# Optimization experiments

Measured on AMD Instinct MI355X. Metric: run time of the kernel, lower is better.

## Reference

```python
import jax, jax.numpy as jnp
import numpy as np

EPS = 1e-8
CG_TOL = 1e-4
S_SIGMA = 8   # bilateral grid spatial downsampling
N_BINS = 9    # bilateral grid range bins (intensity in [0,1])


def _conv2d(x, k):
    # x [C,H,W], k [kh,kw] -> same-padded cross-correlation, per channel
    kh, kw = k.shape
    out = jax.lax.conv_general_dilated(x[:, None], k[None, None], (1, 1),
                                       [(kh // 2, kh // 2), (kw // 2, kw // 2)])
    return out[:, 0]


def _conv2d_T(x, k):
    return _conv2d(x, k[::-1, ::-1])


def _conv_bank(x, ks):
    # x [C,H,W], ks [N,kh,kw] -> [N,C,H,W]
    n, kh, kw = ks.shape
    out = jax.lax.conv_general_dilated(x[:, None], ks[:, None], (1, 1),
                                       [(kh // 2, kh // 2), (kw // 2, kw // 2)])
    return out.transpose(1, 0, 2, 3)


def _conv_bank_T(v, ks):
    # v [N,C,H,W] -> sum_n conv(v[n], flip(ks[n])) : [C,H,W]
    n, kh, kw = ks.shape
    lhs = v.transpose(1, 0, 2, 3)          # [C,N,H,W]
    rhs = ks[:, ::-1, ::-1][None]          # [1,N,kh,kw]
    out = jax.lax.conv_general_dilated(lhs, rhs, (1, 1),
                                       [(kh // 2, kh // 2), (kw // 2, kw // 2)])
    return out[:, 0]


def _deconv_grad(blurred, x, kernel, dkw, dks, rkw, rks, rpow, reg_targets):
    # gradient of E(x) = sum_i dkw_i ||dk_i * (k*x - b)||^2
    #                  + sum_j rkw_j sum |rk_j*x - t_j|^{p_j}
    Kx = _conv2d(x, kernel) - blurred
    d = _conv_bank(Kx, dks)                                    # [Nd,C,H,W]
    g = _conv2d_T(_conv_bank_T(2.0 * dkw[:, None, None, None] * d, dks), kernel)
    v = _conv_bank(x, rks) - reg_targets                       # [Nr,C,H,W]
    av = jnp.abs(v) + EPS
    phi = jnp.sign(v) * av ** (rpow[:, None, None, None] - 1.0)
    g = g + _conv_bank_T(rkw[:, None, None, None] * rpow[:, None, None, None] * phi, rks)
    return g


def _deconv_alpha(blurred, x, kernel, dkw, dks, rkw, rks, rpow, reg_targets, p):
    # exact line search for the quadratic part, Gauss-Newton for |.|^p prior
    g = _deconv_grad(blurred, x, kernel, dkw, dks, rkw, rks, rpow, reg_targets)
    num = -jnp.sum(g * p)
    Kp = _conv2d(p, kernel)
    dKp = _conv_bank(Kp, dks)
    den = jnp.sum(2.0 * dkw[:, None, None, None] * dKp ** 2)
    v = _conv_bank(x, rks) - reg_targets
    Rp = _conv_bank(p, rks)
    w = (rkw * rpow * (rpow - 1.0))[:, None, None, None]
    den = den + jnp.sum(w * (jnp.abs(v) + EPS) ** (rpow[:, None, None, None] - 2.0) * Rp ** 2)
    return num / (den + 1e-12)


def _deconv_prior(x, rks, thr):
    # soft-shrinkage of filtered responses -> regularization targets
    v = _conv_bank(x, rks)
    return jnp.sign(v) * jnp.maximum(jnp.abs(v) - thr[:, None, None, None], 0.0)


def _conv_axis(g, f, axis):
    k = f.shape[0]; r = k // 2; L = g.shape[axis]
    pad = [(0, 0)] * g.ndim; pad[axis] = (r, r)
    gp = jnp.pad(g, pad)
    out = jnp.zeros_like(g)
    for t in range(k):  # fixed small tap count
        out = out + f[t] * jax.lax.slice_in_dim(gp, t, t + L, axis=axis)
    return out


def _bilateral_channel(I, fs, fr):
    # learned-filter bilateral grid: splat -> separable filter (fs,fs,fr) -> trilinear slice
    H, W = I.shape
    gh, gw = H // S_SIGMA, W // S_SIGMA
    Ic = jnp.clip(I, 0.0, 1.0)
    yy, xx = jnp.meshgrid(jnp.arange(H), jnp.arange(W), indexing="ij")
    yi = yy // S_SIGMA; xi = xx // S_SIGMA
    zi = jnp.clip(jnp.round(Ic * (N_BINS - 1)).astype(jnp.int32), 0, N_BINS - 1)
    flat = ((yi * gw + xi) * N_BINS + zi).ravel()
    gv = jnp.zeros(gh * gw * N_BINS, Ic.dtype).at[flat].add(Ic.ravel())
    gw_ = jnp.zeros(gh * gw * N_BINS, Ic.dtype).at[flat].add(1.0)
    g2 = jnp.stack([gv, gw_], -1).reshape(gh, gw, N_BINS, 2)
    g2 = _conv_axis(_conv_axis(_conv_axis(g2, fs, 0), fs, 1), fr, 2)
    yf = yy / S_SIGMA; xf = xx / S_SIGMA; zf = Ic * (N_BINS - 1)

    def corners(f, n):
        c0 = jnp.clip(jnp.floor(f).astype(jnp.int32), 0, n - 1)
        c1 = jnp.minimum(c0 + 1, n - 1)
        w = jnp.clip(f - c0, 0.0, 1.0)
        return c0, c1, w

    y0, y1, wy = corners(yf, gh)
    x0, x1, wx = corners(xf, gw)
    z0, z1, wz = corners(zf, N_BINS)
    acc = jnp.zeros(I.shape + (2,), Ic.dtype)
    for yc, wyc in ((y0, 1 - wy), (y1, wy)):
        for xc, wxc in ((x0, 1 - wx), (x1, wx)):
            for zc, wzc in ((z0, 1 - wz), (z1, wz)):
                acc = acc + (wyc * wxc * wzc)[..., None] * g2[yc, xc, zc]
    return acc[..., 0] / (acc[..., 1] + 1e-8)


def _forward(blurred_batch, kernel_batch, data_kernels, data_kernel_weights,
             reg_kernels, reg_kernel_weights, reg_powers, filter_s, filter_r,
             reg_thresholds, num_cg_iter):
    num_stages = filter_s.shape[0]
    n_reg = reg_kernels.shape[1]

    def single(blurred, kernel):
        def cg(x, idx, reg_targets):
            dkw = data_kernel_weights[idx]; dks = data_kernels[idx]
            rkw = reg_kernel_weights[idx]; rks = reg_kernels[idx]; rp = reg_powers[idx]
            g = _deconv_grad(blurred, x, kernel, dkw, dks, rkw, rks, rp, reg_targets)
            r = -g
            r_norm = jnp.sum(r * r)
            r0 = r_norm

            def body(i, carry):
                x, r, p, rn, done = carry
                alpha = _deconv_alpha(blurred, x, kernel, dkw, dks, rkw, rks, rp, reg_targets, p)
                x1 = x + alpha * p
                g1 = _deconv_grad(blurred, x1, kernel, dkw, dks, rkw, rks, rp, reg_targets)
                r1 = -g1
                nrn = jnp.sum(r1 * r1)
                beta = nrn / (rn + 1e-20)
                conv_now = nrn < CG_TOL * r0
                p1 = r1 + beta * p
                x_n = jnp.where(done, x, x1)
                r_n = jnp.where(done, r, r1)
                rn_n = jnp.where(done, rn, nrn)
                p_n = jnp.where(done | conv_now, p, p1)
                return (x_n, r_n, p_n, rn_n, done | conv_now)

            carry = (x, r, r, r_norm, jnp.array(False))
            x, _, _, _, _ = jax.lax.fori_loop(0, num_cg_iter, body, carry)
            return x

        x = cg(blurred, 0, jnp.zeros((n_reg,) + blurred.shape, blurred.dtype))
        for stage in range(num_stages):
            x = jax.vmap(lambda ch: _bilateral_channel(ch, filter_s[stage], filter_r[stage]))(x)
            reg_targets = _deconv_prior(x, reg_kernels[stage + 1], reg_thresholds[stage])
            x = cg(x, stage + 1, reg_targets)
        return x

    return jax.vmap(single)(blurred_batch, kernel_batch)


def setup_inputs() -> dict:
    key = jax.random.key(0)
    k1, k2 = jax.random.split(key)
    B, C, H, W, KS = 2, 3, 512, 512, 15
    blurred = jax.random.uniform(k1, (B, C, H, W), jnp.float32)
    kern = jax.random.uniform(k2, (B, KS, KS), jnp.float32)
    kern = kern / jnp.sum(kern, axis=(1, 2), keepdims=True)  # normalized PSFs

    ns = 1; c = 2  # num_stages, kernel center (5x5)
    rk = np.zeros((ns + 1, 5, 5, 5), np.float32)
    rk[:, 0, c, c] = -1.0; rk[:, 0, c + 1, c] = 1.0
    rk[:, 1, c, c] = -1.0; rk[:, 1, c, c + 1] = 1.0
    rk[:, 2, c, c] = 1.0; rk[:, 2, c + 1, c] = -1.0
    rk[:, 2, c, c + 1] = -1.0; rk[:, 2, c + 1, c + 1] = 1.0
    rk[:, 3, c - 1, c] = 1.0; rk[:, 3, c, c] = -2.0; rk[:, 3, c + 1, c] = 1.0
    rk[:, 4, c, c - 1] = 1.0; rk[:, 4, c, c] = -2.0; rk[:, 4, c, c + 1] = 1.0
    dk = np.zeros((ns + 1, 6, 5, 5), np.float32)
    dk[:, 0, c, c] = 1.0
    dk[:, 1:] = rk
    dkw = np.zeros((ns + 1, 6), np.float32); dkw[:, 0] = 1.0
    rkw = np.zeros((ns + 1, 5), np.float32)
    rkw[0, :] = 0.001; rkw[1:, :] = 0.05
    rpow = np.full((ns + 1, 5), 2.0, np.float32)
    fs = np.zeros((ns, 11), np.float32); fs[:, 3:8] = [0.0, 1.0, 2.0, 1.0, 0.0]
    fr = np.tile(np.array([0.0, 1.0, 2.0, 1.0, 0.0], np.float32), (ns, 1))
    thr = np.tile(np.array([0.065, 0.065, 0.0325, 0.0325, 0.0325], np.float32), (ns, 1))

    return {
        "blurred_batch": blurred,
        "kernel_batch": kern,
        "data_kernels": jnp.asarray(dk),
        "data_kernel_weights": jnp.asarray(dkw),
        "reg_kernels": jnp.asarray(rk),
        "reg_kernel_weights": jnp.asarray(rkw),
        "reg_powers": jnp.asarray(rpow),
        "filter_s": jnp.asarray(fs),
        "filter_r": jnp.asarray(fr),
        "reg_thresholds": jnp.asarray(thr),
        "num_cg_iter": 5,
    }


def reference(blurred_batch, kernel_batch, data_kernels, data_kernel_weights,
              reg_kernels, reg_kernel_weights, reg_powers, filter_s, filter_r,
              reg_thresholds, num_cg_iter):
    return _forward(blurred_batch, kernel_batch, data_kernels, data_kernel_weights,
                    reg_kernels, reg_kernel_weights, reg_powers, filter_s, filter_r,
                    reg_thresholds, num_cg_iter)
```

## Files before the change

kernel.cpp:

```cpp
#include <hip/hip_runtime.h>

constexpr int Bn = 2, Cn = 3, Hh = 512, Ww = 512;
constexpr int KS = 15, KR = 7;
constexpr int NDK = 6, NRK = 5;
constexpr int GH = 64, GW = 64, NBn = 9, SS = 8;
constexpr float EPSf = 1e-8f;
constexpr float CGTOL = 1e-4f;
constexpr int PLANE = Hh * Ww;
constexpr int CHW = Cn * PLANE;
constexpr int BX = 64, BY = 16;
constexpr int GXc = Ww / BX, GYc = Hh / BY;
constexpr int PB = GXc * GYc * Cn;
constexpr int SA = 80, THt = 30;
constexpr int S2W = 72, S2H = 24;
constexpr int PHW = 68, PHH = 20;
constexpr int PHG = (PHW / 4) * PHH;
constexpr int NITER = 5;

struct CgState { float alpha, beta, rn, r0; int done, pflag; int pad0, pad1; };

struct SolveInfo {
    int fastBank;
    int allrp2;
    int nd;
// ... 38 lines not shown
                    acc += ch * rks_i[m * 25 + ay * 5 + ax] * rks_i[m * 25 + by * 5 + bx];
                }
        }
        s->C[t] = acc;
    }
    if (t == 81) {
        int fast = 1, nd = 0; float tot = 0.f;
        for (int n = 0; n < NDK; n++) {
            if (dkw_i[n] == 0.f) continue;
            int cnt = 0, pos = -1;
            for (int q = 0; q < 25; q++) if (dks_i[n * 25 + q] != 0.f) { cnt++; pos = q; }
            if (cnt > 1) fast = 0;
            if (cnt == 1 && nd < NDK) {
                float v = dks_i[n * 25 + pos];
                s->dsc[nd] = 2.f * dkw_i[n] * v * v;
                s->ddy[nd] = pos / 5 - 2; s->ddx[nd] = pos % 5 - 2;
                tot += s->dsc[nd]; nd++;
            }
        }
        s->fastBank = fast; s->nd = fast ? nd : 0; s->sctot = tot;
    }
    if (t == 82) {
        int ok = 1;
        for (int m = 0; m < NRK; m++) {
            float wm = rkw_i[m], rp = rpw_i[m];
            if (wm != 0.f && rp != 2.f && wm * rp * (rp - 1.f) != 0.f) ok = 0;
        }
        s->allrp2 = ok;
    }
}

__global__ __launch_bounds__(256)
void k_conv15(const float* __restrict__ src, const float* __restrict__ rb,
              const float* __restrict__ pbuf, float* __restrict__ xcopy,
              const float* __restrict__ sub, float* __restrict__ out,
              const float* __restrict__ kernB, float* __restrict__ part,
              const SolveInfo* __restrict__ si,
              const CgState* __restrict__ st, const int* __restrict__ ncg,
              int iter, int mode)
{
    const int pz = blockIdx.z, b = pz / Cn, c = pz % Cn;
    const CgState s = st[b];
    if (mode == 2 && (s.done != 0 || iter >= *ncg)) return;
    __shared__ __align__(16) float tile[SA * THt];
    __shared__ float red[256];
    const int tx = threadIdx.x, ty = threadIdx.y, tid = ty * 16 + tx;
    const int ox0 = blockIdx.x * BX, oy0 = blockIdx.y * BY;
    const int baseP = pz * PLANE;
    const float beta = s.beta; const int pf = s.pflag;
    const float* kp = kernB + b * 225;

    float nm = 0.f;
    for (int i = tid; i < 78 * THt; i += 256) {
        int ly = i / 78, lx = i % 78;
        int gy = oy0 - KR + ly, gx = ox0 - KR + lx;
        float v = 0.f;
        if (gy >= 0 && gy < Hh && gx >= 0 && gx < Ww) {
            int gi = baseP + gy * Ww + gx;
            if (mode == 2) {
                float rv = rb[gi], pv = pbuf[gi];
                v = pf ? fmaf(beta, pv, rv) : pv;
                if (ly >= KR && ly < KR + BY && lx >= KR && lx < KR + BX)
                    nm = fmaf(rv, v, nm);
            } else {
                v = src[gi];
                if (mode == 0 && ly >= KR && ly < KR + BY && lx >= KR && lx < KR + BX)
                    xcopy[gi] = v;
            }
        }
        tile[ly * SA + lx] = v;
    }
    __syncthreads();

    const int colbase = tx * 4;
    float a0 = 0.f, a1 = 0.f, a2 = 0.f, a3 = 0.f;
    for (int i = 0; i < KS; i++) {
        const float4* rp4 = reinterpret_cast<const float4*>(&tile[(ty + i) * SA + colbase]);
        float f[20];
        #pragma unroll
        for (int s5 = 0; s5 < 5; s5++) {
            float4 w4 = rp4[s5];
            f[s5 * 4] = w4.x; f[s5 * 4 + 1] = w4.y; f[s5 * 4 + 2] = w4.z; f[s5 * 4 + 3] = w4.w;
        }
        const float* kr = kp + i * 15;
        #pragma unroll
        for (int j = 0; j < KS; j++) {
            float kv = kr[j];
            a0 = fmaf(kv, f[j], a0); a1 = fmaf(kv, f[j + 1], a1);
            a2 = fmaf(kv, f[j + 2], a2); a3 = fmaf(kv, f[j + 3], a3);
        }
    }
    const int gi = baseP + (oy0 + ty) * Ww + ox0 + colbase;
    if (sub) {
        float4 sv = *reinterpret_cast<const float4*>(&sub[gi]);
        a0 -= sv.x; a1 -= sv.y; a2 -= sv.z; a3 -= sv.w;
    }
    if (si->fastBank) {
        const int gy = oy0 + ty, gx0 = ox0 + colbase;
        if (gy >= 2 && gy <= Hh - 3 && gx0 >= 2 && gx0 + 3 <= Ww - 3) {
            float sc = si->sctot;
// ... 83 lines not shown
            if (!gyin || gx0 + 3 < 0 || gx0 + 3 >= Ww) v3 = 0.f;
            *reinterpret_cast<float4*>(&dl[zy * PHW + zx0]) = make_float4(v0, v1, v2, v3);
        }
        __syncthreads();
        float c0 = 0.f, c1 = 0.f, c2 = 0.f, c3 = 0.f;
        #pragma unroll
        for (int a = 0; a < 5; a++) {
            int fr = 4 - a;
            bool rz = dnr[fr*5]==0.f && dnr[fr*5+1]==0.f && dnr[fr*5+2]==0.f &&
                      dnr[fr*5+3]==0.f && dnr[fr*5+4]==0.f;
            if (rz) continue;
            const float4* q4 = reinterpret_cast<const float4*>(&dl[(ty + a) * PHW + colbase]);
            float4 u0 = q4[0], u1 = q4[1];
            float f8[8] = {u0.x,u0.y,u0.z,u0.w,u1.x,u1.y,u1.z,u1.w};
            #pragma unroll
            for (int bb = 0; bb < 5; bb++) {
                float kv = dnr[fr * 5 + (4 - bb)];
                if (kv != 0.f) {
                    c0 = fmaf(kv, f8[bb], c0); c1 = fmaf(kv, f8[bb+1], c1);
                    c2 = fmaf(kv, f8[bb+2], c2); c3 = fmaf(kv, f8[bb+3], c3);
                }
            }
        }
        t0 = fmaf(wn, c0, t0); t1 = fmaf(wn, c1, t1);
        t2 = fmaf(wn, c2, t2); t3 = fmaf(wn, c3, t3);
        __syncthreads();
    }
    const int gi = baseP + (oy0 + ty) * Ww + ox0 + colbase;
    *reinterpret_cast<float4*>(&tbuf[gi]) = make_float4(t0, t1, t2, t3);
}

__global__ __launch_bounds__(256)
void k_hess(const float* __restrict__ kx, const float* __restrict__ wb,
            const float* __restrict__ rb, const float* __restrict__ pbuf,
            float* __restrict__ qb, const float* __restrict__ kernB,
            const float* __restrict__ rks, const float* __restrict__ rkw,
            const float* __restrict__ rpw, const SolveInfo* __restrict__ si,
            float* __restrict__ part, const CgState* __restrict__ st,
            const int* __restrict__ ncg, int iter)
{
    if (!si->allrp2) return;
    const int pz = blockIdx.z, b = pz / Cn, c = pz % Cn;
    const CgState s = st[b];
    if (s.done != 0 || iter >= *ncg) return;
    __shared__ __align__(16) float wt[SA * THt];
    __shared__ __align__(16) float s2[S2W * S2H];
    __shared__ __align__(16) float sC[81];
    __shared__ float rk5[NRK * 25];
    __shared__ float srkw[NRK], srpw[NRK];
    __shared__ float red[256];
    float* ph = wt;
    const int tx = threadIdx.x, ty = threadIdx.y, tid = ty * 16 + tx;
    const int ox0 = blockIdx.x * BX, oy0 = blockIdx.y * BY;
    const int baseP = pz * PLANE;
    const float beta = s.beta; const int pf = s.pflag;
    const float* wsrc = si->fastBank ? kx : wb;
    const float* kp = kernB + b * 225;

    for (int i = tid; i < 81; i += 256) sC[i] = si->C[i];
    for (int i = tid; i < NRK * 25; i += 256) rk5[i] = rks[i];
    if (tid < NRK) { srkw[tid] = rkw[tid]; srpw[tid] = rpw[tid]; }

    for (int i = tid; i < 78 * THt; i += 256) {
        int ly = i / 78, lx = i % 78;
        int gy = oy0 - KR + ly, gx = ox0 - KR + lx;
        wt[ly * SA + lx] = (gy >= 0 && gy < Hh && gx >= 0 && gx < Ww)
                           ? wsrc[baseP + gy * Ww + gx] : 0.f;
    }
    for (int i = tid; i < S2W * S2H; i += 256) {
        int ly = i / S2W, lx = i % S2W;
        int gy = oy0 - 4 + ly, gx = ox0 - 4 + lx;
        float v = 0.f;
        if (gy >= 0 && gy < Hh && gx >= 0 && gx < Ww) {
            int gi = baseP + gy * Ww + gx;
            float rv = rb[gi], pv = pbuf[gi];
            v = pf ? fmaf(beta, pv, rv) : pv;
        }
        s2[i] = v;
    }
    __syncthreads();

    const int colbase = tx * 4;
    float a0 = 0.f, a1 = 0.f, a2 = 0.f, a3 = 0.f;
    for (int i = 0; i < KS; i++) {
        const float4* rp4 = reinterpret_cast<const float4*>(&wt[(ty + i) * SA + colbase]);
        float f[20];
        #pragma unroll
        for (int s5 = 0; s5 < 5; s5++) {
            float4 w4 = rp4[s5];
            f[s5 * 4] = w4.x; f[s5 * 4 + 1] = w4.y; f[s5 * 4 + 2] = w4.z; f[s5 * 4 + 3] = w4.w;
        }
        const float* kr = kp + (14 - i) * 15;
        #pragma unroll
        for (int j = 0; j < KS; j++) {
            float kv = kr[14 - j];
            a0 = fmaf(kv, f[j], a0); a1 = fmaf(kv, f[j + 1], a1);
            a2 = fmaf(kv, f[j + 2], a2); a3 = fmaf(kv, f[j + 3], a3);
        }
    }

    const bool blkInterior = (oy0 >= 2) && (oy0 + BY - 1 <= Hh - 3) &&
                             (ox0 >= 2) && (ox0 + BX - 1 <= Ww - 3);
    if (blkInterior) {
        #pragma unroll
        for (int oy = 0; oy < 9; oy++) {
            float cr[9]; bool nz = false;
            #pragma unroll
            for (int ox = 0; ox < 9; ox++) { cr[ox] = sC[oy * 9 + ox]; nz = nz || (cr[ox] != 0.f); }
            if (!nz) continue;
            const float4* s4 = reinterpret_cast<const float4*>(&s2[(ty + oy) * S2W + colbase]);
            float4 u0 = s4[0], u1 = s4[1], u2 = s4[2];
// ... 54 lines not shown
                if (rz) continue;
                const float4* q4 = reinterpret_cast<const float4*>(&ph[(ty + a) * PHW + colbase]);
                float4 u0 = q4[0], u1 = q4[1];
                float f8[8] = {u0.x,u0.y,u0.z,u0.w,u1.x,u1.y,u1.z,u1.w};
                #pragma unroll
                for (int bb = 0; bb < 5; bb++) {
                    float kv = rmr[fr * 5 + (4 - bb)];
                    if (kv != 0.f) {
                        a0 = fmaf(kv, f8[bb], a0); a1 = fmaf(kv, f8[bb+1], a1);
                        a2 = fmaf(kv, f8[bb+2], a2); a3 = fmaf(kv, f8[bb+3], a3);
                    }
                }
            }
            __syncthreads();
        }
    }

    const int gy = oy0 + ty, gx0 = ox0 + colbase;
    const int gi = baseP + gy * Ww + gx0;
    *reinterpret_cast<float4*>(&qb[gi]) = make_float4(a0, a1, a2, a3);
    int li = (ty + 4) * S2W + colbase + 4;
    float redv = s2[li] * a0 + s2[li + 1] * a1 + s2[li + 2] * a2 + s2[li + 3] * a3;
    float tot = blockReduce(redv, red, tid);
    if (tid == 0) {
        int blk = c * (GXc * GYc) + blockIdx.y * GXc + blockIdx.x;
        part[((size_t)b * 4 + 1) * PB + blk] = tot;
    }
}

__global__ __launch_bounds__(256)
void k_gradL(const float* __restrict__ kx, const float* __restrict__ wb,
             const float* __restrict__ xg,
             const float* __restrict__ rb, const float* __restrict__ pbuf,
             const float* __restrict__ tgt, float* __restrict__ outb,
             float* __restrict__ pout, const float* __restrict__ kernB,
             const float* __restrict__ rks, const float* __restrict__ rkw,
             const float* __restrict__ rpw, const SolveInfo* __restrict__ si,
             float* __restrict__ part, const CgState* __restrict__ st,
             const int* __restrict__ ncg, int iter, int mode)
{
    if (mode == 1 && si->allrp2) return;
    const int pz = blockIdx.z, b = pz / Cn, c = pz % Cn;
    const CgState s = st[b];
    if (mode == 1 && (s.done != 0 || iter >= *ncg)) return;
    __shared__ __align__(16) float wt[SA * THt];
    __shared__ __align__(16) float s2[S2W * S2H];
    __shared__ float rk5[NRK * 25];
    __shared__ float srkw[NRK], srpw[NRK];
    __shared__ float red[256];
    float* ph = wt;
    const int tx = threadIdx.x, ty = threadIdx.y, tid = ty * 16 + tx;
    const int ox0 = blockIdx.x * BX, oy0 = blockIdx.y * BY;
    const int baseP = pz * PLANE;
    const float beta = s.beta; const int pf = s.pflag;
    const float* wsrc = si->fastBank ? kx : wb;
    const float* kp = kernB + b * 225;

    for (int i = tid; i < NRK * 25; i += 256) rk5[i] = rks[i];
    if (tid < NRK) { srkw[tid] = rkw[tid]; srpw[tid] = rpw[tid]; }

    for (int i = tid; i < 78 * THt; i += 256) {
        int ly = i / 78, lx = i % 78;
        int gy = oy0 - KR + ly, gx = ox0 - KR + lx;
        wt[ly * SA + lx] = (gy >= 0 && gy < Hh && gx >= 0 && gx < Ww)
                           ? wsrc[baseP + gy * Ww + gx] : 0.f;
    }
    for (int i = tid; i < S2W * S2H; i += 256) {
        int ly = i / S2W, lx = i % S2W;
        int gy = oy0 - 4 + ly, gx = ox0 - 4 + lx;
        float v = 0.f;
        if (gy >= 0 && gy < Hh && gx >= 0 && gx < Ww) {
            int gi = baseP + gy * Ww + gx;
            if (mode == 0) v = xg[gi];
            else { float rv = rb[gi], pv = pbuf[gi]; v = pf ? fmaf(beta, pv, rv) : pv; }
        }
        s2[i] = v;
    }
    __syncthreads();

    const int colbase = tx * 4;
    float a0 = 0.f, a1 = 0.f, a2 = 0.f, a3 = 0.f;
    for (int i = 0; i < KS; i++) {
        const float4* rp4 = reinterpret_cast<const float4*>(&wt[(ty + i) * SA + colbase]);
        float f[20];
        #pragma unroll
        for (int s5 = 0; s5 < 5; s5++) {
            float4 w4 = rp4[s5];
            f[s5 * 4] = w4.x; f[s5 * 4 + 1] = w4.y; f[s5 * 4 + 2] = w4.z; f[s5 * 4 + 3] = w4.w;
        }
        const float* kr = kp + (14 - i) * 15;
        #pragma unroll
        for (int j = 0; j < KS; j++) {
            float kv = kr[14 - j];
            a0 = fmaf(kv, f[j], a0); a1 = fmaf(kv, f[j + 1], a1);
            a2 = fmaf(kv, f[j + 2], a2); a3 = fmaf(kv, f[j + 3], a3);
        }
    }
    __syncthreads();

    for (int m = 0; m < NRK; m++) {
        float wm = srkw[m], rp = srpw[m];
        if (wm == 0.f) continue;
        float rmr[25];
        #pragma unroll
        for (int q = 0; q < 25; q++) rmr[q] = rk5[m * 25 + q];
        const float* tgm = tgt ? tgt + ((size_t)(b * NRK + m)) * CHW + (size_t)c * PLANE : nullptr;
        const float coefG = wm * rp;
        const float coefH = wm * rp * (rp - 1.f);

        for (int t = tid; t < PHG; t += 256) {
            int zy = t / 17, zx0 = (t % 17) * 4;
            int gy = oy0 - 2 + zy, gx0 = ox0 - 2 + zx0;
            float v0 = 0.f, v1 = 0.f, v2 = 0.f, v3 = 0.f;
            #pragma unroll
            for (int a = 0; a < 5; a++) {
                bool rz = rmr[a*5]==0.f && rmr[a*5+1]==0.f && rmr[a*5+2]==0.f &&
                          rmr[a*5+3]==0.f && rmr[a*5+4]==0.f;
                if (rz) continue;
                const float4* s4 = reinterpret_cast<const float4*>(&s2[(zy + a) * S2W + zx0]);
                float4 u0 = s4[0], u1 = s4[1];
                float f8[8] = {u0.x,u0.y,u0.z,u0.w,u1.x,u1.y,u1.z,u1.w};
                #pragma unroll
                for (int bb = 0; bb < 5; bb++) {
                    float kv = rmr[a * 5 + bb];
                    if (kv != 0.f) {
                        v0 = fmaf(kv, f8[bb], v0); v1 = fmaf(kv, f8[bb+1], v1);
                        v2 = fmaf(kv, f8[bb+2], v2); v3 = fmaf(kv, f8[bb+3], v3);
                    }
                }
            }
            bool gyin = (gy >= 0 && gy < Hh);
            float o0 = 0.f, o1 = 0.f, o2 = 0.f, o3 = 0.f;
            #pragma unroll
            for (int j = 0; j < 4; j++) {
                int gx = gx0 + j;
                if (!gyin || gx < 0 || gx >= Ww) continue;
                float v = (j == 0) ? v0 : (j == 1) ? v1 : (j == 2) ? v2 : v3;
                float o;
                if (mode == 0) {
                    if (tgm) v -= tgm[gy * Ww + gx];
                    float sg = (v > 0.f) ? 1.f : ((v < 0.f) ? -1.f : 0.f);
                    float av = fabsf(v) + EPSf;
                    o = coefG * sg * ((rp == 2.f) ? av : powf(av, rp - 1.f));
                } else {
                    float fac = 1.f;
                    if (rp != 2.f) {
                        float vx = 0.f;
                        for (int a = 0; a < 5; a++)
                            for (int bb = 0; bb < 5; bb++) {
                                int yy = gy - 2 + a, xx = gx - 2 + bb;
                                if (yy >= 0 && yy < Hh && xx >= 0 && xx < Ww)
                                    vx = fmaf(rmr[a * 5 + bb], xg[baseP + yy * Ww + xx], vx);
                            }
                        if (tgm) vx -= tgm[gy * Ww + gx];
                        fac = powf(fabsf(vx) + EPSf, rp - 2.f);
                    }
                    o = coefH * fac * v;
                }
                if (j == 0) o0 = o; else if (j == 1) o1 = o; else if (j == 2) o2 = o; else o3 = o;
            }
            *reinterpret_cast<float4*>(&ph[zy * PHW + zx0]) = make_float4(o0, o1, o2, o3);
        }
        __syncthreads();
        #pragma unroll
        for (int a = 0; a < 5; a++) {
            int fr = 4 - a;
            bool rz = rmr[fr*5]==0.f && rmr[fr*5+1]==0.f && rmr[fr*5+2]==0.f &&
                      rmr[fr*5+3]==0.f && rmr[fr*5+4]==0.f;
            if (rz) continue;
            const float4* q4 = reinterpret_cast<const float4*>(&ph[(ty + a) * PHW + colbase]);
            float4 u0 = q4[0], u1 = q4[1];
            float f8[8] = {u0.x,u0.y,u0.z,u0.w,u1.x,u1.y,u1.z,u1.w};
            #pragma unroll
            for (int bb = 0; bb < 5; bb++) {
                float kv = rmr[fr * 5 + (4 - bb)];
                if (kv != 0.f) {
                    a0 = fmaf(kv, f8[bb], a0); a1 = fmaf(kv, f8[bb+1], a1);
                    a2 = fmaf(kv, f8[bb+2], a2); a3 = fmaf(kv, f8[bb+3], a3);
                }
            }
        }
        __syncthreads();
    }

    const int gi = baseP + (oy0 + ty) * Ww + ox0 + colbase;
    float redv;
    if (mode == 0) {
        float r0v = -a0, r1v = -a1, r2v = -a2, r3v = -a3;
        float4 rv4 = make_float4(r0v, r1v, r2v, r3v);
        *reinterpret_cast<float4*>(&outb[gi]) = rv4;
        *reinterpret_cast<float4*>(&pout[gi]) = rv4;
        redv = r0v * r0v + r1v * r1v + r2v * r2v + r3v * r3v;
    } else {
        *reinterpret_cast<float4*>(&outb[gi]) = make_float4(a0, a1, a2, a3);
        int li = (ty + 4) * S2W + colbase + 4;
        redv = s2[li] * a0 + s2[li + 1] * a1 + s2[li + 2] * a2 + s2[li + 3] * a3;
    }
    float tot = blockReduce(redv, red, tid);
    if (tid == 0) {
        int blk = c * (GXc * GYc) + blockIdx.y * GXc + blockIdx.x;
        int slot = (mode == 0) ? 2 : 1;
        part[((size_t)b * 4 + slot) * PB + blk] = tot;
    }
}

__global__ __launch_bounds__(256)
void k_axpy(float4* __restrict__ x, float4* __restrict__ r, float4* __restrict__ p,
            const float4* __restrict__ q, float* __restrict__ part,
            const CgState* __restrict__ st, const int* __restrict__ ncg, int iter)
{
    const int b = blockIdx.y;
    const CgState s = st[b];
    if (s.done != 0 || iter >= *ncg) return;
    __shared__ float red[256];
    const int tid = threadIdx.x;
    const int idx = b * (CHW / 4) + blockIdx.x * 256 + tid;
    float4 pv = p[idx], rv = r[idx], qv = q[idx], xv = x[idx];
    float4 pc;
    if (s.pflag) {
        pc.x = fmaf(s.beta, pv.x, rv.x); pc.y = fmaf(s.beta, pv.y, rv.y);
        pc.z = fmaf(s.beta, pv.z, rv.z); pc.w = fmaf(s.beta, pv.w, rv.w);
    } else pc = pv;
    xv.x = fmaf(s.alpha, pc.x, xv.x); xv.y = fmaf(s.alpha, pc.y, xv.y);
    xv.z = fmaf(s.alpha, pc.z, xv.z); xv.w = fmaf(s.alpha, pc.w, xv.w);
    rv.x = fmaf(-s.alpha, qv.x, rv.x); rv.y = fmaf(-s.alpha, qv.y, rv.y);
    rv.z = fmaf(-s.alpha, qv.z, rv.z); rv.w = fmaf(-s.alpha, qv.w, rv.w);
    x[idx] = xv; r[idx] = rv; p[idx] = pc;
    float nr = rv.x * rv.x + rv.y * rv.y + rv.z * rv.z + rv.w * rv.w;
    float tot = blockReduce(nr, red, tid);
    if (tid == 0) part[((size_t)b * 4 + 2) * PB + blockIdx.x] = tot;
}

__global__ __launch_bounds__(256)
void k_fin_alpha(const float* __restrict__ part, CgState* st,
                 const int* __restrict__ ncg, int iter)
{
    const int b = blockIdx.x, tid = threadIdx.x;
    __shared__ float red[256];
    if (st[b].done != 0 || iter >= *ncg) { if (tid == 0) st[b].alpha = 0.f; return; }
    float sn = 0.f, sd = 0.f;
    for (int i = tid; i < PB; i += 256) {
        sn += part[((size_t)b * 4 + 0) * PB + i];
        sd += part[((size_t)b * 4 + 1) * PB + i];
    }
    float num = blockReduce(sn, red, tid);
    float den = blockReduce(sd, red, tid);
    if (tid == 0) st[b].alpha = num / (den + 1e-12f);
}

__global__ __launch_bounds__(256)
void k_fin_iter(const float* __restrict__ part, CgState* st,
                const int* __restrict__ ncg, int iter, int mode)
{
    const int b = blockIdx.x, tid = threadIdx.x;
    __shared__ float red[256];
    if (mode == 1 && (st[b].done != 0 || iter >= *ncg)) { if (tid == 0) st[b].pflag = 0; return; }
    float s = 0.f;
    for (int i = tid; i < PB; i += 256) s += part[((size_t)b * 4 + 2) * PB + i];
    float nrn = blockReduce(s, red, tid);
    if (tid == 0) {
// ... 64 lines not shown
void k_slice(const float* __restrict__ xin, const float* __restrict__ grid,
             float* __restrict__ xout)
{
    const int pz = blockIdx.z;
    const int id = blockIdx.x * 256 + threadIdx.x;
    const int py = id / Ww, px = id % Ww;
    float I = xin[(size_t)pz * PLANE + id];
    float Ic = fminf(fmaxf(I, 0.f), 1.f);
    float yf = (float)py / SS, xf = (float)px / SS, zf = Ic * (NBn - 1);
    int y0 = min(max((int)floorf(yf), 0), GH - 1); int y1 = min(y0 + 1, GH - 1);
    float wy = fminf(fmaxf(yf - (float)y0, 0.f), 1.f);
    int x0 = min(max((int)floorf(xf), 0), GW - 1); int x1 = min(x0 + 1, GW - 1);
    float wx = fminf(fmaxf(xf - (float)x0, 0.f), 1.f);
    int z0 = min(max((int)floorf(zf), 0), NBn - 1); int z1 = min(z0 + 1, NBn - 1);
    float wz = fminf(fmaxf(zf - (float)z0, 0.f), 1.f);
    const float* gp = grid + (size_t)pz * GH * GW * NBn * 2;
    const int   ys[2] = { y0, y1 };  const float wys[2] = { 1.f - wy, wy };
    const int   xs[2] = { x0, x1 };  const float wxs[2] = { 1.f - wx, wx };
    const int   zs[2] = { z0, z1 };  const float wzs[2] = { 1.f - wz, wz };
    float a0 = 0.f, a1 = 0.f;
    for (int iy = 0; iy < 2; iy++)
        for (int ix = 0; ix < 2; ix++)
            for (int iz = 0; iz < 2; iz++) {
                float w = wys[iy] * wxs[ix] * wzs[iz];
                size_t idx = (((size_t)ys[iy] * GW + xs[ix]) * NBn + zs[iz]) * 2;
                a0 = fmaf(w, gp[idx], a0);
                a1 = fmaf(w, gp[idx + 1], a1);
            }
    xout[(size_t)pz * PLANE + id] = a0 / (a1 + 1e-8f);
}

__global__ __launch_bounds__(256)
void k_prior(const float* __restrict__ x, float* __restrict__ tgt,
             const float* __restrict__ rks, const float* __restrict__ thr)
{
    const int pz = blockIdx.z, b = pz / Cn, c = pz % Cn;
    __shared__ float xl[24 * 24];
    __shared__ float rkk[NRK * 25];
    __shared__ float sthr[NRK];
    const int tx = threadIdx.x, ty = threadIdx.y, tid = ty * 16 + tx;
    const int ox0 = blockIdx.x * 16, oy0 = blockIdx.y * 16;
    const int baseP = pz * PLANE;
    for (int i = tid; i < NRK * 25; i += 256) rkk[i] = rks[i];
    if (tid < NRK) sthr[tid] = thr[tid];
    for (int i = tid; i < 24 * 24; i += 256) {
        int ly = i / 24, lx = i % 24;
        int gy = oy0 - 2 + ly, gx = ox0 - 2 + lx;
        xl[i] = (gy >= 0 && gy < Hh && gx >= 0 && gx < Ww) ? x[baseP + gy * Ww + gx] : 0.f;
    }
    __syncthreads();
    const int pix = (oy0 + ty) * Ww + (ox0 + tx);
    for (int m = 0; m < NRK; m++) {
        const float* rm = &rkk[m * 25];
        float v = 0.f;
        #pragma unroll
        for (int a = 0; a < 5; a++)
            #pragma unroll
            for (int bb = 0; bb < 5; bb++)
                v = fmaf(rm[a * 5 + bb], xl[(ty + a) * 24 + (tx + bb)], v);
        float sg = (v > 0.f) ? 1.f : ((v < 0.f) ? -1.f : 0.f);
        tgt[((size_t)(b * NRK + m)) * CHW + (size_t)c * PLANE + pix] =
            sg * fmaxf(fabsf(v) - sthr[m], 0.f);
    }
}

extern "C" void kernel_launch(void* const* d_in, const int* in_sizes, int n_in,
                              void* d_out, int out_size, void* d_ws, size_t ws_size,
                              hipStream_t stream)
{
    const float* blurred = (const float*)d_in[0];
    const float* kern    = (const float*)d_in[1];
    const float* dks     = (const float*)d_in[2];
    const float* dkw     = (const float*)d_in[3];
    const float* rks     = (const float*)d_in[4];
    const float* rkw     = (const float*)d_in[5];
    const float* rpw     = (const float*)d_in[6];
    const float* fs      = (const float*)d_in[7];
    const float* fr      = (const float*)d_in[8];
    const float* thr     = (const float*)d_in[9];
    const int*   ncg     = (const int*)d_in[10];
    (void)in_sizes; (void)n_in; (void)out_size; (void)ws_size;

    float* w = (float*)d_ws;
    size_t off = 0;
    auto alloc = [&](size_t n) { float* p = w + off; off += n; return p; };
    float* xb   = alloc((size_t)Bn * CHW);
    float* pbuf = alloc((size_t)Bn * CHW);
    float* rbuf = alloc((size_t)Bn * CHW);
    float* kx   = alloc((size_t)Bn * CHW);
    float* wb   = alloc((size_t)Bn * CHW);
    float* qb   = alloc((size_t)Bn * CHW);
    float* tg   = alloc((size_t)Bn * NRK * CHW);
    float* g0   = alloc((size_t)Bn * Cn * GH * GW * NBn * 2);
    float* g1   = alloc((size_t)Bn * Cn * GH * GW * NBn * 2);
    float* part = alloc((size_t)Bn * 4 * PB);
    CgState* st = (CgState*)(w + off); off += Bn * 8;
    SolveInfo* sinf = (SolveInfo*)(w + off); off += 2 * ((sizeof(SolveInfo) + 3) / 4);

    dim3 tb(16, 16), grd(GXc, GYc, Bn * Cn);

    k_comp<<<2, 128, 0, stream>>>(dkw, dks, rkw, rpw, rks, sinf);

    auto solve = [&](int idx, const float* tgt, int initmode) {
        const float* dks_i = dks + (size_t)idx * NDK * 25;
        const float* dkw_i = dkw + (size_t)idx * NDK;
        const float* rks_i = rks + (size_t)idx * NRK * 25;
        const float* rkw_i = rkw + (size_t)idx * NRK;
        const float* rpw_i = rpw + (size_t)idx * NRK;
        const SolveInfo* si = sinf + idx;
        k_conv15<<<grd, tb, 0, stream>>>(initmode == 0 ? blurred : xb, nullptr, nullptr,
                                         initmode == 0 ? xb : nullptr, blurred, kx, kern,
                                         nullptr, si, st, ncg, 0, initmode == 0 ? 0 : 3);
        k_bank<<<grd, tb, 0, stream>>>(kx, wb, dks_i, dkw_i, si, st, ncg, 0, 0);
        k_gradL<<<grd, tb, 0, stream>>>(kx, wb, xb, nullptr, nullptr, tgt, rbuf, pbuf, kern,
                                        rks_i, rkw_i, rpw_i, si, part, st, ncg, 0, 0);
        k_fin_iter<<<Bn, 256, 0, stream>>>(part, st, ncg, 0, 0);
        for (int i = 0; i < NITER; i++) {
            k_conv15<<<grd, tb, 0, stream>>>(nullptr, rbuf, pbuf, nullptr, nullptr, kx, kern,
                                             part, si, st, ncg, i, 2);
            k_bank<<<grd, tb, 0, stream>>>(kx, wb, dks_i, dkw_i, si, st, ncg, i, 1);
            k_hess<<<grd, tb, 0, stream>>>(kx, wb, rbuf, pbuf, qb, kern,
                                           rks_i, rkw_i, rpw_i, si, part, st, ncg, i);
            k_gradL<<<grd, tb, 0, stream>>>(kx, wb, xb, rbuf, pbuf, tgt, qb, nullptr, kern,
                                            rks_i, rkw_i, rpw_i, si, part, st, ncg, i, 1);
            k_fin_alpha<<<Bn, 256, 0, stream>>>(part, st, ncg, i);
            k_axpy<<<dim3(PB, Bn), 256, 0, stream>>>((float4*)xb, (float4*)rbuf, (float4*)pbuf,
                                                     (const float4*)qb, part, st, ncg, i);
            k_fin_iter<<<Bn, 256, 0, stream>>>(part, st, ncg, i, 1);
        }
    };

    solve(0, nullptr, 0);

    dim3 sb(8, 8), sg(GW, GH, Bn * Cn);
    k_splat<<<sg, sb, 0, stream>>>(xb, g0);
    const int totalg = Bn * Cn * GH * GW * NBn;
    k_blur<<<(totalg + 255) / 256, 256, 0, stream>>>(g0, g1, fs, 11, 0);
    k_blur<<<(totalg + 255) / 256, 256, 0, stream>>>(g1, g0, fs, 11, 1);
    k_blur<<<(totalg + 255) / 256, 256, 0, stream>>>(g0, g1, fr, 5, 2);
    k_slice<<<dim3(PLANE / 256, 1, Bn * Cn), 256, 0, stream>>>(xb, g1, xb);

    k_prior<<<dim3(Ww / 16, Hh / 16, Bn * Cn), tb, 0, stream>>>(xb, tg, rks + NRK * 25, thr);

    solve(1, tg, 1);

    hipMemcpyAsync(d_out, xb, (size_t)Bn * CHW * sizeof(float),
                   hipMemcpyDeviceToDevice, stream);
}
```

Before: 1.364 ms.

## Materialize CG direction once, fuse prior targets into gradient, add interior fast path

The conv15 kernel now writes the updated search direction p = r + beta*p into a ping-pong buffer, so hess and axpy read it directly instead of recomputing it from r and p. When all prior powers are 2, the prior-target kernel is skipped and the thresholded prior term is computed inside the gradient kernel. Interior blocks in the first solve use a precomputed 9x9 combined stencil in place of the two-pass 5x5 bank. This adds a buffer and more branching in the gradient kernel, and the mode-0 prior term now takes its values from a different source.

```diff
diff --git a/kernel.cpp b/kernel.cpp
--- a/kernel.cpp
+++ b/kernel.cpp
@@ -94,7 +94,7 @@
 
 __global__ __launch_bounds__(256)
 void k_conv15(const float* __restrict__ src, const float* __restrict__ rb,
-              const float* __restrict__ pbuf, float* __restrict__ xcopy,
+              const float* __restrict__ pbuf, float* __restrict__ aux2,
               const float* __restrict__ sub, float* __restrict__ out,
               const float* __restrict__ kernB, float* __restrict__ part,
               const SolveInfo* __restrict__ si,
@@ -122,12 +122,14 @@
             if (mode == 2) {
                 float rv = rb[gi], pv = pbuf[gi];
                 v = pf ? fmaf(beta, pv, rv) : pv;
-                if (ly >= KR && ly < KR + BY && lx >= KR && lx < KR + BX)
+                if (ly >= KR && ly < KR + BY && lx >= KR && lx < KR + BX) {
                     nm = fmaf(rv, v, nm);
+                    aux2[gi] = v;
+                }
             } else {
                 v = src[gi];
                 if (mode == 0 && ly >= KR && ly < KR + BY && lx >= KR && lx < KR + BX)
-                    xcopy[gi] = v;
+                    aux2[gi] = v;
             }
         }
         tile[ly * SA + lx] = v;
@@ -277,7 +279,7 @@
 
 __global__ __launch_bounds__(256)
 void k_hess(const float* __restrict__ kx, const float* __restrict__ wb,
-            const float* __restrict__ rb, const float* __restrict__ pbuf,
+            const float* __restrict__ pn,
             float* __restrict__ qb, const float* __restrict__ kernB,
             const float* __restrict__ rks, const float* __restrict__ rkw,
             const float* __restrict__ rpw, const SolveInfo* __restrict__ si,
@@ -298,7 +300,6 @@
     const int tx = threadIdx.x, ty = threadIdx.y, tid = ty * 16 + tx;
     const int ox0 = blockIdx.x * BX, oy0 = blockIdx.y * BY;
     const int baseP = pz * PLANE;
-    const float beta = s.beta; const int pf = s.pflag;
     const float* wsrc = si->fastBank ? kx : wb;
     const float* kp = kernB + b * 225;
 
@@ -315,13 +316,8 @@
     for (int i = tid; i < S2W * S2H; i += 256) {
         int ly = i / S2W, lx = i % S2W;
         int gy = oy0 - 4 + ly, gx = ox0 - 4 + lx;
-        float v = 0.f;
-        if (gy >= 0 && gy < Hh && gx >= 0 && gx < Ww) {
-            int gi = baseP + gy * Ww + gx;
-            float rv = rb[gi], pv = pbuf[gi];
-            v = pf ? fmaf(beta, pv, rv) : pv;
-        }
-        s2[i] = v;
+        s2[i] = (gy >= 0 && gy < Hh && gx >= 0 && gx < Ww)
+                ? pn[baseP + gy * Ww + gx] : 0.f;
     }
     __syncthreads();
 
@@ -442,7 +438,8 @@
 void k_gradL(const float* __restrict__ kx, const float* __restrict__ wb,
              const float* __restrict__ xg,
              const float* __restrict__ rb, const float* __restrict__ pbuf,
-             const float* __restrict__ tgt, float* __restrict__ outb,
+             const float* __restrict__ tgt, const float* __restrict__ thr,
+             float* __restrict__ outb,
              float* __restrict__ pout, const float* __restrict__ kernB,
              const float* __restrict__ rks, const float* __restrict__ rkw,
              const float* __restrict__ rpw, const SolveInfo* __restrict__ si,
@@ -455,8 +452,9 @@
     if (mode == 1 && (s.done != 0 || iter >= *ncg)) return;
     __shared__ __align__(16) float wt[SA * THt];
     __shared__ __align__(16) float s2[S2W * S2H];
+    __shared__ __align__(16) float sC[81];
     __shared__ float rk5[NRK * 25];
-    __shared__ float srkw[NRK], srpw[NRK];
+    __shared__ float srkw[NRK], srpw[NRK], sthr[NRK];
     __shared__ float red[256];
     float* ph = wt;
     const int tx = threadIdx.x, ty = threadIdx.y, tid = ty * 16 + tx;
@@ -466,8 +464,12 @@
     const float* wsrc = si->fastBank ? kx : wb;
     const float* kp = kernB + b * 225;
 
+    for (int i = tid; i < 81; i += 256) sC[i] = si->C[i];
     for (int i = tid; i < NRK * 25; i += 256) rk5[i] = rks[i];
-    if (tid < NRK) { srkw[tid] = rkw[tid]; srpw[tid] = rpw[tid]; }
+    if (tid < NRK) {
+        srkw[tid] = rkw[tid]; srpw[tid] = rpw[tid];
+        sthr[tid] = thr ? thr[tid] : 0.f;
+    }
 
     for (int i = tid; i < 78 * THt; i += 256) {
         int ly = i / 78, lx = i % 78;
@@ -506,91 +508,119 @@
             a2 = fmaf(kv, f[j + 2], a2); a3 = fmaf(kv, f[j + 3], a3);
         }
     }
-    __syncthreads();
-
-    for (int m = 0; m < NRK; m++) {
-        float wm = srkw[m], rp = srpw[m];
-        if (wm == 0.f) continue;
-        float rmr[25];
-        #pragma unroll
-        for (int q = 0; q < 25; q++) rmr[q] = rk5[m * 25 + q];
-        const float* tgm = tgt ? tgt + ((size_t)(b * NRK + m)) * CHW + (size_t)c * PLANE : nullptr;
-        const float coefG = wm * rp;
-        const float coefH = wm * rp * (rp - 1.f);
-
-        for (int t = tid; t < PHG; t += 256) {
-            int zy = t / 17, zx0 = (t % 17) * 4;
-            int gy = oy0 - 2 + zy, gx0 = ox0 - 2 + zx0;
-            float v0 = 0.f, v1 = 0.f, v2 = 0.f, v3 = 0.f;
+
+    const bool blkInterior = (oy0 >= 2) && (oy0 + BY - 1 <= Hh - 3) &&
+                             (ox0 >= 2) && (ox0 + BX - 1 <= Ww - 3);
+    if (mode == 0 && si->allrp2 && thr == nullptr && blkInterior) {
+        #pragma unroll
+        for (int oy = 0; oy < 9; oy++) {
+            float cr[9]; bool nz = false;
+            #pragma unroll
+            for (int ox = 0; ox < 9; ox++) { cr[ox] = sC[oy * 9 + ox]; nz = nz || (cr[ox] != 0.f); }
+            if (!nz) continue;
+            const float4* s4 = reinterpret_cast<const float4*>(&s2[(ty + oy) * S2W + colbase]);
+            float4 u0 = s4[0], u1 = s4[1], u2 = s4[2];
+            float f12[12] = {u0.x,u0.y,u0.z,u0.w,u1.x,u1.y,u1.z,u1.w,u2.x,u2.y,u2.z,u2.w};
+            #pragma unroll
+            for (int ox = 0; ox < 9; ox++) {
+                float kv = cr[ox];
+                if (kv != 0.f) {
+                    a0 = fmaf(kv, f12[ox], a0); a1 = fmaf(kv, f12[ox + 1], a1);
+                    a2 = fmaf(kv, f12[ox + 2], a2); a3 = fmaf(kv, f12[ox + 3], a3);
+                }
+            }
+        }
+    } else {
+        __syncthreads();
+        for (int m = 0; m < NRK; m++) {
+            float wm = srkw[m], rp = srpw[m];
+            if (wm == 0.f) continue;
+            float rmr[25];
+            #pragma unroll
+            for (int q = 0; q < 25; q++) rmr[q] = rk5[m * 25 + q];
+            const float* tgm = (mode == 1 && tgt)
+                ? tgt + ((size_t)(b * NRK + m)) * CHW + (size_t)c * PLANE : nullptr;
+            const float coefG = wm * rp;
+            const float coefH = wm * rp * (rp - 1.f);
+            const float thrm = sthr[m];
+
+            for (int t = tid; t < PHG; t += 256) {
+                int zy = t / 17, zx0 = (t % 17) * 4;
+                int gy = oy0 - 2 + zy, gx0 = ox0 - 2 + zx0;
+                float v0 = 0.f, v1 = 0.f, v2 = 0.f, v3 = 0.f;
+                #pragma unroll
+                for (int a = 0; a < 5; a++) {
+                    bool rz = rmr[a*5]==0.f && rmr[a*5+1]==0.f && rmr[a*5+2]==0.f &&
+                              rmr[a*5+3]==0.f && rmr[a*5+4]==0.f;
+                    if (rz) continue;
+                    const float4* s4 = reinterpret_cast<const float4*>(&s2[(zy + a) * S2W + zx0]);
+                    float4 u0 = s4[0], u1 = s4[1];
+                    float f8[8] = {u0.x,u0.y,u0.z,u0.w,u1.x,u1.y,u1.z,u1.w};
+                    #pragma unroll
+                    for (int bb = 0; bb < 5; bb++) {
+                        float kv = rmr[a * 5 + bb];
+                        if (kv != 0.f) {
+                            v0 = fmaf(kv, f8[bb], v0); v1 = fmaf(kv, f8[bb+1], v1);
+                            v2 = fmaf(kv, f8[bb+2], v2); v3 = fmaf(kv, f8[bb+3], v3);
+                        }
+                    }
+                }
+                bool gyin = (gy >= 0 && gy < Hh);
+                float o0 = 0.f, o1 = 0.f, o2 = 0.f, o3 = 0.f;
+                #pragma unroll
+                for (int j = 0; j < 4; j++) {
+                    int gx = gx0 + j;
+                    if (!gyin || gx < 0 || gx >= Ww) continue;
+                    float v = (j == 0) ? v0 : (j == 1) ? v1 : (j == 2) ? v2 : v3;
+                    float o;
+                    if (mode == 0) {
+                        if (thr) {
+                            float sgv = (v > 0.f) ? 1.f : ((v < 0.f) ? -1.f : 0.f);
+                            v = sgv * fminf(fabsf(v), thrm);
+                        }
+                        float sg = (v > 0.f) ? 1.f : ((v < 0.f) ? -1.f : 0.f);
+                        float av = fabsf(v) + EPSf;
+                        o = coefG * sg * ((rp == 2.f) ? av : powf(av, rp - 1.f));
+                    } else {
+                        float fac = 1.f;
+                        if (rp != 2.f) {
+                            float vx = 0.f;
+                            for (int a = 0; a < 5; a++)
+                                for (int bb = 0; bb < 5; bb++) {
+                                    int yy = gy - 2 + a, xx = gx - 2 + bb;
+                                    if (yy >= 0 && yy < Hh && xx >= 0 && xx < Ww)
+                                        vx = fmaf(rmr[a * 5 + bb], xg[baseP + yy * Ww + xx], vx);
+                                }
+                            if (tgm) vx -= tgm[gy * Ww + gx];
+                            fac = powf(fabsf(vx) + EPSf, rp - 2.f);
+                        }
+                        o = coefH * fac * v;
+                    }
+                    if (j == 0) o0 = o; else if (j == 1) o1 = o; else if (j == 2) o2 = o; else o3 = o;
+                }
+                *reinterpret_cast<float4*>(&ph[zy * PHW + zx0]) = make_float4(o0, o1, o2, o3);
+            }
+            __syncthreads();
             #pragma unroll
             for (int a = 0; a < 5; a++) {
-                bool rz = rmr[a*5]==0.f && rmr[a*5+1]==0.f && rmr[a*5+2]==0.f &&
-                          rmr[a*5+3]==0.f && rmr[a*5+4]==0.f;
+                int fr = 4 - a;
+                bool rz = rmr[fr*5]==0.f && rmr[fr*5+1]==0.f && rmr[fr*5+2]==0.f &&
+                          rmr[fr*5+3]==0.f && rmr[fr*5+4]==0.f;
                 if (rz) continue;
-                const float4* s4 = reinterpret_cast<const float4*>(&s2[(zy + a) * S2W + zx0]);
-                float4 u0 = s4[0], u1 = s4[1];
+                const float4* q4 = reinterpret_cast<const float4*>(&ph[(ty + a) * PHW + colbase]);
+                float4 u0 = q4[0], u1 = q4[1];
                 float f8[8] = {u0.x,u0.y,u0.z,u0.w,u1.x,u1.y,u1.z,u1.w};
                 #pragma unroll
                 for (int bb = 0; bb < 5; bb++) {
-                    float kv = rmr[a * 5 + bb];
+                    float kv = rmr[fr * 5 + (4 - bb)];
                     if (kv != 0.f) {
-                        v0 = fmaf(kv, f8[bb], v0); v1 = fmaf(kv, f8[bb+1], v1);
-                        v2 = fmaf(kv, f8[bb+2], v2); v3 = fmaf(kv, f8[bb+3], v3);
+                        a0 = fmaf(kv, f8[bb], a0); a1 = fmaf(kv, f8[bb+1], a1);
+                        a2 = fmaf(kv, f8[bb+2], a2); a3 = fmaf(kv, f8[bb+3], a3);
                     }
                 }
             }
-            bool gyin = (gy >= 0 && gy < Hh);
-            float o0 = 0.f, o1 = 0.f, o2 = 0.f, o3 = 0.f;
-            #pragma unroll
-            for (int j = 0; j < 4; j++) {
-                int gx = gx0 + j;
-                if (!gyin || gx < 0 || gx >= Ww) continue;
-                float v = (j == 0) ? v0 : (j == 1) ? v1 : (j == 2) ? v2 : v3;
-                float o;
-                if (mode == 0) {
-                    if (tgm) v -= tgm[gy * Ww + gx];
-                    float sg = (v > 0.f) ? 1.f : ((v < 0.f) ? -1.f : 0.f);
-                    float av = fabsf(v) + EPSf;
-                    o = coefG * sg * ((rp == 2.f) ? av : powf(av, rp - 1.f));
-                } else {
-                    float fac = 1.f;
-                    if (rp != 2.f) {
-                        float vx = 0.f;
-                        for (int a = 0; a < 5; a++)
-                            for (int bb = 0; bb < 5; bb++) {
-                                int yy = gy - 2 + a, xx = gx - 2 + bb;
-                                if (yy >= 0 && yy < Hh && xx >= 0 && xx < Ww)
-                                    vx = fmaf(rmr[a * 5 + bb], xg[baseP + yy * Ww + xx], vx);
-                            }
-                        if (tgm) vx -= tgm[gy * Ww + gx];
-                        fac = powf(fabsf(vx) + EPSf, rp - 2.f);
-                    }
-                    o = coefH * fac * v;
-                }
-                if (j == 0) o0 = o; else if (j == 1) o1 = o; else if (j == 2) o2 = o; else o3 = o;
-            }
-            *reinterpret_cast<float4*>(&ph[zy * PHW + zx0]) = make_float4(o0, o1, o2, o3);
-        }
-        __syncthreads();
-        #pragma unroll
-        for (int a = 0; a < 5; a++) {
-            int fr = 4 - a;
-            bool rz = rmr[fr*5]==0.f && rmr[fr*5+1]==0.f && rmr[fr*5+2]==0.f &&
-                      rmr[fr*5+3]==0.f && rmr[fr*5+4]==0.f;
-            if (rz) continue;
-            const float4* q4 = reinterpret_cast<const float4*>(&ph[(ty + a) * PHW + colbase]);
-            float4 u0 = q4[0], u1 = q4[1];
-            float f8[8] = {u0.x,u0.y,u0.z,u0.w,u1.x,u1.y,u1.z,u1.w};
-            #pragma unroll
-            for (int bb = 0; bb < 5; bb++) {
-                float kv = rmr[fr * 5 + (4 - bb)];
-                if (kv != 0.f) {
-                    a0 = fmaf(kv, f8[bb], a0); a1 = fmaf(kv, f8[bb+1], a1);
-                    a2 = fmaf(kv, f8[bb+2], a2); a3 = fmaf(kv, f8[bb+3], a3);
-                }
-            }
-        }
-        __syncthreads();
+            __syncthreads();
+        }
     }
 
     const int gi = baseP + (oy0 + ty) * Ww + ox0 + colbase;
@@ -615,7 +645,8 @@
 }
 
 __global__ __launch_bounds__(256)
-void k_axpy(float4* __restrict__ x, float4* __restrict__ r, float4* __restrict__ p,
+void k_axpy(float4* __restrict__ x, float4* __restrict__ r,
+            const float4* __restrict__ pn,
             const float4* __restrict__ q, float* __restrict__ part,
             const CgState* __restrict__ st, const int* __restrict__ ncg, int iter)
 {
@@ -625,17 +656,12 @@
     __shared__ float red[256];
     const int tid = threadIdx.x;
     const int idx = b * (CHW / 4) + blockIdx.x * 256 + tid;
-    float4 pv = p[idx], rv = r[idx], qv = q[idx], xv = x[idx];
-    float4 pc;
-    if (s.pflag) {
-        pc.x = fmaf(s.beta, pv.x, rv.x); pc.y = fmaf(s.beta, pv.y, rv.y);
-        pc.z = fmaf(s.beta, pv.z, rv.z); pc.w = fmaf(s.beta, pv.w, rv.w);
-    } else pc = pv;
+    float4 pc = pn[idx], rv = r[idx], qv = q[idx], xv = x[idx];
     xv.x = fmaf(s.alpha, pc.x, xv.x); xv.y = fmaf(s.alpha, pc.y, xv.y);
     xv.z = fmaf(s.alpha, pc.z, xv.z); xv.w = fmaf(s.alpha, pc.w, xv.w);
     rv.x = fmaf(-s.alpha, qv.x, rv.x); rv.y = fmaf(-s.alpha, qv.y, rv.y);
     rv.z = fmaf(-s.alpha, qv.z, rv.z); rv.w = fmaf(-s.alpha, qv.w, rv.w);
-    x[idx] = xv; r[idx] = rv; p[idx] = pc;
+    x[idx] = xv; r[idx] = rv;
     float nr = rv.x * rv.x + rv.y * rv.y + rv.z * rv.z + rv.w * rv.w;
     float tot = blockReduce(nr, red, tid);
     if (tid == 0) part[((size_t)b * 4 + 2) * PB + blockIdx.x] = tot;
@@ -766,8 +792,10 @@
 
 __global__ __launch_bounds__(256)
 void k_prior(const float* __restrict__ x, float* __restrict__ tgt,
-             const float* __restrict__ rks, const float* __restrict__ thr)
-{
+             const float* __restrict__ rks, const float* __restrict__ thr,
+             const SolveInfo* __restrict__ si)
+{
+    if (si->allrp2) return;
     const int pz = blockIdx.z, b = pz / Cn, c = pz % Cn;
     __shared__ float xl[24 * 24];
     __shared__ float rkk[NRK * 25];
@@ -818,16 +846,17 @@
     float* w = (float*)d_ws;
     size_t off = 0;
     auto alloc = [&](size_t n) { float* p = w + off; off += n; return p; };
-    float* xb   = alloc((size_t)Bn * CHW);
-    float* pbuf = alloc((size_t)Bn * CHW);
-    float* rbuf = alloc((size_t)Bn * CHW);
-    float* kx   = alloc((size_t)Bn * CHW);
-    float* wb   = alloc((size_t)Bn * CHW);
-    float* qb   = alloc((size_t)Bn * CHW);
-    float* tg   = alloc((size_t)Bn * NRK * CHW);
-    float* g0   = alloc((size_t)Bn * Cn * GH * GW * NBn * 2);
-    float* g1   = alloc((size_t)Bn * Cn * GH * GW * NBn * 2);
-    float* part = alloc((size_t)Bn * 4 * PB);
+    float* xb    = alloc((size_t)Bn * CHW);
+    float* pbufA = alloc((size_t)Bn * CHW);
+    float* pbufB = alloc((size_t)Bn * CHW);
+    float* rbuf  = alloc((size_t)Bn * CHW);
+    float* kx    = alloc((size_t)Bn * CHW);
+    float* wb    = alloc((size_t)Bn * CHW);
+    float* qb    = alloc((size_t)Bn * CHW);
+    float* tg    = alloc((size_t)Bn * NRK * CHW);
+    float* g0    = alloc((size_t)Bn * Cn * GH * GW * NBn * 2);
+    float* g1    = alloc((size_t)Bn * Cn * GH * GW * NBn * 2);
+    float* part  = alloc((size_t)Bn * 4 * PB);
     CgState* st = (CgState*)(w + off); off += Bn * 8;
     SolveInfo* sinf = (SolveInfo*)(w + off); off += 2 * ((sizeof(SolveInfo) + 3) / 4);
 
@@ -835,7 +864,7 @@
 
     k_comp<<<2, 128, 0, stream>>>(dkw, dks, rkw, rpw, rks, sinf);
 
-    auto solve = [&](int idx, const float* tgt, int initmode) {
+    auto solve = [&](int idx, const float* tgt, const float* thr_i, int initmode) {
         const float* dks_i = dks + (size_t)idx * NDK * 25;
         const float* dkw_i = dkw + (size_t)idx * NDK;
         const float* rks_i = rks + (size_t)idx * NRK * 25;
@@ -846,25 +875,30 @@
                                          initmode == 0 ? xb : nullptr, blurred, kx, kern,
                                          nullptr, si, st, ncg, 0, initmode == 0 ? 0 : 3);
         k_bank<<<grd, tb, 0, stream>>>(kx, wb, dks_i, dkw_i, si, st, ncg, 0, 0);
-        k_gradL<<<grd, tb, 0, stream>>>(kx, wb, xb, nullptr, nullptr, tgt, rbuf, pbuf, kern,
+        k_gradL<<<grd, tb, 0, stream>>>(kx, wb, xb, nullptr, nullptr, tgt, thr_i,
+                                        rbuf, pbufA, kern,
                                         rks_i, rkw_i, rpw_i, si, part, st, ncg, 0, 0);
         k_fin_iter<<<Bn, 256, 0, stream>>>(part, st, ncg, 0, 0);
+        float* pcur = pbufA;
+        float* pnxt = pbufB;
         for (int i = 0; i < NITER; i++) {
-            k_conv15<<<grd, tb, 0, stream>>>(nullptr, rbuf, pbuf, nullptr, nullptr, kx, kern,
+            k_conv15<<<grd, tb, 0, stream>>>(nullptr, rbuf, pcur, pnxt, nullptr, kx, kern,
                                              part, si, st, ncg, i, 2);
             k_bank<<<grd, tb, 0, stream>>>(kx, wb, dks_i, dkw_i, si, st, ncg, i, 1);
-            k_hess<<<grd, tb, 0, stream>>>(kx, wb, rbuf, pbuf, qb, kern,
+            k_hess<<<grd, tb, 0, stream>>>(kx, wb, pnxt, qb, kern,
                                            rks_i, rkw_i, rpw_i, si, part, st, ncg, i);
-            k_gradL<<<grd, tb, 0, stream>>>(kx, wb, xb, rbuf, pbuf, tgt, qb, nullptr, kern,
+            k_gradL<<<grd, tb, 0, stream>>>(kx, wb, xb, rbuf, pnxt, tgt, thr_i, qb, nullptr, kern,
                                             rks_i, rkw_i, rpw_i, si, part, st, ncg, i, 1);
             k_fin_alpha<<<Bn, 256, 0, stream>>>(part, st, ncg, i);
-            k_axpy<<<dim3(PB, Bn), 256, 0, stream>>>((float4*)xb, (float4*)rbuf, (float4*)pbuf,
+            k_axpy<<<dim3(PB, Bn), 256, 0, stream>>>((float4*)xb, (float4*)rbuf,
+                                                     (const float4*)pnxt,
                                                      (const float4*)qb, part, st, ncg, i);
             k_fin_iter<<<Bn, 256, 0, stream>>>(part, st, ncg, i, 1);
+            float* tswap = pcur; pcur = pnxt; pnxt = tswap;
         }
     };
 
-    solve(0, nullptr, 0);
+    solve(0, nullptr, nullptr, 0);
 
     dim3 sb(8, 8), sg(GW, GH, Bn * Cn);
     k_splat<<<sg, sb, 0, stream>>>(xb, g0);
@@ -874,9 +908,10 @@
     k_blur<<<(totalg + 255) / 256, 256, 0, stream>>>(g0, g1, fr, 5, 2);
     k_slice<<<dim3(PLANE / 256, 1, Bn * Cn), 256, 0, stream>>>(xb, g1, xb);
 
-    k_prior<<<dim3(Ww / 16, Hh / 16, Bn * Cn), tb, 0, stream>>>(xb, tg, rks + NRK * 25, thr);
-
-    solve(1, tg, 1);
+    k_prior<<<dim3(Ww / 16, Hh / 16, Bn * Cn), tb, 0, stream>>>(xb, tg, rks + NRK * 25, thr,
+                                                                sinf + 1);
+
+    solve(1, tg, thr, 1);
 
     hipMemcpyAsync(d_out, xb, (size_t)Bn * CHW * sizeof(float),
                    hipMemcpyDeviceToDevice, stream);
```

Measured after the change: 1.337 ms. -2.0%, faster.
